# Optimization experiments

Measured on AMD Instinct MI355X. Metric: run time of the kernel, lower is better.

## Reference

```python
import jax, jax.numpy as jnp
import numpy as np

DIM = 768
NUM_HEADS = 12
HEAD_DIM = DIM // NUM_HEADS
HW = 32  # input_size = (32, 32)


def setup_inputs() -> dict:
    key = jax.random.key(0)
    ks = jax.random.split(key, 7)
    return {
        "x": jax.random.normal(ks[0], (8, HW, HW, DIM), dtype=jnp.float32),
        "w_qkv": jax.random.normal(ks[1], (DIM, 3 * DIM), dtype=jnp.float32) * 0.02,
        "b_qkv": jnp.zeros((3 * DIM,), dtype=jnp.float32),
        "w_proj": jax.random.normal(ks[2], (DIM, DIM), dtype=jnp.float32) * 0.02,
        "b_proj": jnp.zeros((DIM,), dtype=jnp.float32),
        "rel_pos_h": jax.random.normal(ks[3], (2 * HW - 1, HEAD_DIM), dtype=jnp.float32) * 0.02,
        "rel_pos_w": jax.random.normal(ks[4], (2 * HW - 1, HEAD_DIM), dtype=jnp.float32) * 0.02,
    }


def _gather_rel_pos(size, rel_pos):
    # q_size == k_size == size, so no resize; index = i - j + (size - 1)
    idx = jnp.arange(size)[:, None] - jnp.arange(size)[None, :] + (size - 1)
    return rel_pos[idx]  # [size, size, head_dim]


def reference(x, w_qkv, b_qkv, w_proj, b_proj, rel_pos_h, rel_pos_w):
    B, H, W, C = x.shape
    nH, D = NUM_HEADS, HEAD_DIM
    scale = D ** -0.5
    S = H * W

    qkv = x.reshape(B, S, C) @ w_qkv + b_qkv          # [B,S,3C]
    qkv = qkv.reshape(B, S, 3, nH, D).transpose(2, 0, 3, 1, 4)  # [3,B,nH,S,D]
    q, k, v = qkv[0], qkv[1], qkv[2]

    attn = jnp.einsum('bnsd,bntd->bnst', q * scale, k)  # [B,nH,S,S]

    # decomposed relative positional bias
    Rh = _gather_rel_pos(H, rel_pos_h)                  # [H,H,D]
    Rw = _gather_rel_pos(W, rel_pos_w)                  # [W,W,D]
    r_q = q.reshape(B, nH, H, W, D)
    rel_h = jnp.einsum('bnhwc,hkc->bnhwk', r_q, Rh)     # [B,nH,H,W,H]
    rel_w = jnp.einsum('bnhwc,wkc->bnhwk', r_q, Rw)     # [B,nH,H,W,W]
    attn = (attn.reshape(B, nH, H, W, H, W)
            + rel_h[..., :, None]
            + rel_w[..., None, :]).reshape(B, nH, S, S)

    attn = jax.nn.softmax(attn, axis=-1)
    out = jnp.einsum('bnst,bntd->bnsd', attn, v)        # [B,nH,S,D]
    out = out.transpose(0, 2, 1, 3).reshape(B, H, W, C)
    return out @ w_proj + b_proj
```

## Files before the change

### kernel.cpp

```cpp
#include <hip/hip_runtime.h>
#include <cstdint>
#include <cstddef>

#define NH 12
#define HDIM 64
#define C_ 768
#define C3 2304
#define SEQ 1024
#define LS 72
#define SMAX 6.0f

typedef short bf16x8_t __attribute__((ext_vector_type(8)));
typedef float f32x4_t __attribute__((ext_vector_type(4)));
typedef unsigned short u16x4_t __attribute__((ext_vector_type(4)));

__device__ __forceinline__ unsigned short bf16_rne(float x) {
    unsigned int u = __float_as_uint(x);
    u += 0x7FFFu + ((u >> 16) & 1u);
    return (unsigned short)(u >> 16);
}
__device__ __forceinline__ float bf16f(unsigned short h) {
    return __uint_as_float(((unsigned int)h) << 16);
}

__device__ __forceinline__ void load_lds16(const unsigned short* g, unsigned short* l) {
    auto gp = (const __attribute__((address_space(1))) unsigned short*)(uintptr_t)g;
    auto lp = (__attribute__((address_space(3))) unsigned short*)(uint32_t)(uintptr_t)l;
    __builtin_amdgcn_global_load_lds(gp, lp, 16, 0, 0);
}

__device__ __forceinline__ int swz(int row, int g) {
    const int pr = row >> 1;
    const int ch = (((row & 1) << 2) | g) ^ (pr & 7);
    return pr * 64 + ch * 8;
}

__global__ __launch_bounds__(256)
void split_kernel(const float* __restrict__ in, unsigned short* __restrict__ hi)
{
    const int i = blockIdx.x * 256 + threadIdx.x;
    float4 v = ((const float4*)in)[i];
    u16x4_t h;
    h.x = bf16_rne(v.x); h.y = bf16_rne(v.y); h.z = bf16_rne(v.z); h.w = bf16_rne(v.w);
    ((u16x4_t*)hi)[i] = h;
}

__global__ __launch_bounds__(256)
void splitT_kernel(const float* __restrict__ W, unsigned short* __restrict__ Thi,
                   unsigned short* __restrict__ Tlo, int Kdim, int Ndim)
{
    __shared__ float tile[32][33];
    const int t = threadIdx.x;
    const int kb = blockIdx.y * 32, nb = blockIdx.x * 32;
    const int lr = t >> 3, lc = (t & 7) * 4;
    *(float4*)&tile[lr][lc] = *(const float4*)&W[(size_t)(kb + lr) * Ndim + nb + lc];
    __syncthreads();
    const float v0 = tile[lc + 0][lr];
    const float v1 = tile[lc + 1][lr];
    const float v2 = tile[lc + 2][lr];
    const float v3 = tile[lc + 3][lr];
    u16x4_t h, l;
    h.x = bf16_rne(v0); l.x = bf16_rne(v0 - bf16f(h.x));
    h.y = bf16_rne(v1); l.y = bf16_rne(v1 - bf16f(h.y));
    h.z = bf16_rne(v2); l.z = bf16_rne(v2 - bf16f(h.z));
    h.w = bf16_rne(v3); l.w = bf16_rne(v3 - bf16f(h.w));
    *(u16x4_t*)&Thi[(size_t)(nb + lr) * Kdim + kb + lc] = h;
    *(u16x4_t*)&Tlo[(size_t)(nb + lr) * Kdim + kb + lc] = l;
}

__global__ __launch_bounds__(256, 2)
void qkvgemm_kernel(const unsigned short* __restrict__ Ahi, const unsigned short* __restrict__ BThi,
                    const float* __restrict__ bias,
                    unsigned short* __restrict__ q_hi, unsigned short* __restrict__ k_hi,
                    unsigned short* __restrict__ v_hi)
{
    constexpr int K = 768;
    __shared__ unsigned short As[4096];
    __shared__ unsigned short Bs[4096];
    const int tid = threadIdx.x;
    const int w = tid >> 6, lane = tid & 63, g = lane >> 4, r = lane & 15;
    const int wr = (w >> 1) * 64, wc = (w & 1) * 64;

    const int bid  = blockIdx.x;
    const int xcd  = bid & 7;
    const int idx  = bid >> 3;
    const int msub = idx & 7;
    const int ntile = idx >> 3;
    const int m0 = (xcd * 8 + msub) * 128;
    const int n0 = ntile * 128;

    int row_[2], gc_[2];
#pragma unroll
    for (int i = 0; i < 2; ++i) {
        const int s = i * 256 + tid;
        const int pr = s >> 3;
        const int u = (s & 7) ^ (pr & 7);
        row_[i] = pr * 2 + (u >> 2);
        gc_[i]  = u & 3;
    }
    const unsigned short* gA0 = Ahi + (size_t)(m0 + row_[0]) * K + gc_[0] * 8;
    const unsigned short* gA1 = Ahi + (size_t)(m0 + row_[1]) * K + gc_[1] * 8;
    const unsigned short* gB0 = BThi + (size_t)(n0 + row_[0]) * K + gc_[0] * 8;
    const unsigned short* gB1 = BThi + (size_t)(n0 + row_[1]) * K + gc_[1] * 8;
    unsigned short* lA0 = As + w * 512;
    unsigned short* lA1 = As + 2048 + w * 512;
    unsigned short* lB0 = Bs + w * 512;
    unsigned short* lB1 = Bs + 2048 + w * 512;

    f32x4_t acc[4][4];
#pragma unroll
    for (int i = 0; i < 4; ++i)
#pragma unroll
        for (int j = 0; j < 4; ++j)
#pragma unroll
            for (int q = 0; q < 4; ++q) acc[i][j][q] = 0.f;

    for (int k0 = 0; k0 < K; k0 += 32) {
        __syncthreads();
        load_lds16(gA0 + k0, lA0);
        load_lds16(gA1 + k0, lA1);
        load_lds16(gB0 + k0, lB0);
        load_lds16(gB1 + k0, lB1);
        __syncthreads();
        bf16x8_t am[4];
#pragma unroll
        for (int i = 0; i < 4; ++i)
            am[i] = *(const bf16x8_t*)&As[swz(wr + 16 * i + r, g)];
#pragma unroll
        for (int j = 0; j < 4; ++j) {
            const bf16x8_t bn = *(const bf16x8_t*)&Bs[swz(wc + 16 * j + r, g)];
#pragma unroll
            for (int i = 0; i < 4; ++i)
                acc[i][j] = __builtin_amdgcn_mfma_f32_16x16x32_bf16(am[i], bn, acc[i][j], 0, 0, 0);
        }
    }

    const int third = n0 >= 1536 ? 2 : (n0 >= 768 ? 1 : 0);
    unsigned short* outH = third == 2 ? v_hi : third == 1 ? k_hi : q_hi;
#pragma unroll
    for (int j = 0; j < 4; ++j) {
        const int n = n0 + wc + 16 * j + r;
        const float bj = bias[n];
        const int nn = n - third * 768;
        const int h = nn >> 6, d = nn & 63;
#pragma unroll
        for (int i = 0; i < 4; ++i) {
            const int m = m0 + wr + 16 * i + 4 * g;
            const int b = m >> 10, t = m & 1023;
            const size_t hb = ((size_t)(b * NH + h)) << 16;
            unsigned short* dh = outH + hb + (size_t)t * 64 + d;
#pragma unroll
            for (int q = 0; q < 4; ++q)
                dh[(size_t)q * 64] = bf16_rne(acc[i][j][q] + bj);
        }
    }
}

template<int N>
__global__ __launch_bounds__(256, 2)
void gemm_mfma_kernel(const unsigned short* __restrict__ Ahi, const unsigned short* __restrict__ Alo,
                      const unsigned short* __restrict__ BThi, const unsigned short* __restrict__ BTlo,
                      const float* __restrict__ bias, float* __restrict__ C)
{
    constexpr int K = 768;
    __shared__ unsigned short As[128 * LS];
    __shared__ unsigned short Bs[128 * LS];
    const int tid = threadIdx.x;
    const int w = tid >> 6, lane = tid & 63, g = lane >> 4, r = lane & 15;
    const int wr = (w >> 1) * 64, wc = (w & 1) * 64;

    const int bid  = blockIdx.x;
    const int xcd  = bid & 7;
    const int idx  = bid >> 3;
    const int msub = idx & 7;
    const int ntile = idx >> 3;
    const int m0 = (xcd * 8 + msub) * 128;
    const int n0 = ntile * 128;

    const int srow = tid >> 1, sh = (tid & 1) * 16;

    const unsigned short* aH = Ahi + (size_t)(m0 + srow) * K + sh;
    const unsigned short* aL = Alo + (size_t)(m0 + srow) * K + sh;
    const unsigned short* bH = BThi + (size_t)(n0 + srow) * K + sh;
    const unsigned short* bL = BTlo + (size_t)(n0 + srow) * K + sh;

    f32x4_t acc[4][4];
#pragma unroll
    for (int i = 0; i < 4; ++i)
#pragma unroll
        for (int j = 0; j < 4; ++j)
#pragma unroll
            for (int q = 0; q < 4; ++q) acc[i][j][q] = 0.f;

    for (int k0 = 0; k0 < K; k0 += 32) {
        bf16x8_t va0 = *(const bf16x8_t*)(aH + k0);
        bf16x8_t va1 = *(const bf16x8_t*)(aH + k0 + 8);
        bf16x8_t wa0 = *(const bf16x8_t*)(aL + k0);
        bf16x8_t wa1 = *(const bf16x8_t*)(aL + k0 + 8);
        bf16x8_t vb0 = *(const bf16x8_t*)(bH + k0);
        bf16x8_t vb1 = *(const bf16x8_t*)(bH + k0 + 8);
        bf16x8_t wb0 = *(const bf16x8_t*)(bL + k0);
        bf16x8_t wb1 = *(const bf16x8_t*)(bL + k0 + 8);
        __syncthreads();
        *(bf16x8_t*)&As[srow * LS + sh]          = va0;
        *(bf16x8_t*)&As[srow * LS + sh + 8]      = va1;
        *(bf16x8_t*)&As[srow * LS + 32 + sh]     = wa0;
        *(bf16x8_t*)&As[srow * LS + 32 + sh + 8] = wa1;
        *(bf16x8_t*)&Bs[srow * LS + sh]          = vb0;
        *(bf16x8_t*)&Bs[srow * LS + sh + 8]      = vb1;
        *(bf16x8_t*)&Bs[srow * LS + 32 + sh]     = wb0;
        *(bf16x8_t*)&Bs[srow * LS + 32 + sh + 8] = wb1;
        __syncthreads();
        bf16x8_t amh[4], aml[4];
#pragma unroll
        for (int i = 0; i < 4; ++i) {
            amh[i] = *(const bf16x8_t*)&As[(wr + 16 * i + r) * LS + 8 * g];
            aml[i] = *(const bf16x8_t*)&As[(wr + 16 * i + r) * LS + 32 + 8 * g];
        }
#pragma unroll
        for (int j = 0; j < 4; ++j) {
            bf16x8_t bnh = *(const bf16x8_t*)&Bs[(wc + 16 * j + r) * LS + 8 * g];
            bf16x8_t bnl = *(const bf16x8_t*)&Bs[(wc + 16 * j + r) * LS + 32 + 8 * g];
#pragma unroll
            for (int i = 0; i < 4; ++i) {
                acc[i][j] = __builtin_amdgcn_mfma_f32_16x16x32_bf16(amh[i], bnh, acc[i][j], 0, 0, 0);
                acc[i][j] = __builtin_amdgcn_mfma_f32_16x16x32_bf16(amh[i], bnl, acc[i][j], 0, 0, 0);
                acc[i][j] = __builtin_amdgcn_mfma_f32_16x16x32_bf16(aml[i], bnh, acc[i][j], 0, 0, 0);
            }
        }
    }

#pragma unroll
    for (int j = 0; j < 4; ++j) {
        const float bj = bias[n0 + wc + 16 * j + r];
#pragma unroll
        for (int i = 0; i < 4; ++i) {
            float* Cp = C + (size_t)(m0 + wr + 16 * i + 4 * g) * N + n0 + wc + 16 * j + r;
#pragma unroll
            for (int q = 0; q < 4; ++q)
                Cp[(size_t)q * N] = acc[i][j][q] + bj;
        }
    }
}

__global__ __launch_bounds__(256)
void relcat_kernel(const float* __restrict__ rel_h, const float* __restrict__ rel_w,
                   unsigned short* __restrict__ relcat)
{
    const int i = blockIdx.x * 256 + threadIdx.x;
    if (i >= 2016) return;
    const int j = i * 4;
    const int row = j >> 6, col = j & 63;
    const float* src = row < 63 ? &rel_h[row * 64 + col] : &rel_w[(row - 63) * 64 + col];
    const float4 v = *(const float4*)src;
    u16x4_t h;
    h.x = bf16_rne(v.x); h.y = bf16_rne(v.y); h.z = bf16_rne(v.z); h.w = bf16_rne(v.w);
    *(u16x4_t*)&relcat[j] = h;
}

__global__ __launch_bounds__(256, 4)
void relgemm_kernel(const unsigned short* __restrict__ qhi, const unsigned short* __restrict__ relcat,
                    unsigned short* __restrict__ G)
{
    __shared__ unsigned short bs[128 * LS];
    const int tid = threadIdx.x;
    const int sb = blockIdx.x, bh = blockIdx.y;
    const int w = tid >> 6, lane = tid & 63, g = lane >> 4, r = lane & 15;
    const size_t hb = (size_t)bh << 16;

    {
        const int row = tid >> 1, c32 = (tid & 1) * 32;
        if (row < 126) {
#pragma unroll
            for (int e = 0; e < 4; ++e)
                *(bf16x8_t*)&bs[row * LS + c32 + 8 * e] =
                    *(const bf16x8_t*)&relcat[row * 64 + c32 + 8 * e];
        } else {
            const bf16x8_t z = {0,0,0,0,0,0,0,0};
#pragma unroll
            for (int e = 0; e < 4; ++e)
                *(bf16x8_t*)&bs[row * LS + c32 + 8 * e] = z;
        }
    }
    bf16x8_t aq[2][2];
#pragma unroll
    for (int i = 0; i < 2; ++i)
#pragma unroll
        for (int c = 0; c < 2; ++c)
            aq[i][c] = *(const bf16x8_t*)(qhi + hb + (size_t)(sb * 128 + w * 32 + 16 * i + r) * 64 + c * 32 + 8 * g);
    __syncthreads();

    f32x4_t acc[2][8];
#pragma unroll
    for (int i = 0; i < 2; ++i)
#pragma unroll
        for (int fj = 0; fj < 8; ++fj)
#pragma unroll
            for (int q = 0; q < 4; ++q) acc[i][fj][q] = 0.f;

#pragma unroll
    for (int c = 0; c < 2; ++c)
#pragma unroll
        for (int fj = 0; fj < 8; ++fj) {
            const bf16x8_t brel = *(const bf16x8_t*)&bs[(16 * fj + r) * LS + c * 32 + 8 * g];
#pragma unroll
            for (int i = 0; i < 2; ++i)
                acc[i][fj] = __builtin_amdgcn_mfma_f32_16x16x32_bf16(aq[i][c], brel, acc[i][fj], 0, 0, 0);
        }

    unsigned short* Gb = G + (((size_t)bh << 10) + sb * 128 + w * 32) * 128;
#pragma unroll
    for (int i = 0; i < 2; ++i)
#pragma unroll
        for (int reg = 0; reg < 4; ++reg) {
            unsigned short* Gr = Gb + (size_t)(16 * i + 4 * g + reg) * 128 + r;
#pragma unroll
            for (int fj = 0; fj < 8; ++fj)
                Gr[16 * fj] = bf16_rne(acc[i][fj][reg]);
        }
}

__global__ __launch_bounds__(256, 3)
void attn7_kernel(const unsigned short* __restrict__ qhi,
                  const unsigned short* __restrict__ khi,
                  const unsigned short* __restrict__ vhi,
                  const unsigned short* __restrict__ G,
                  unsigned short* __restrict__ outh, unsigned short* __restrict__ outl)
{
    __shared__ unsigned short ksh[2 * 64 * LS];
    __shared__ unsigned short vsh[2 * 64 * LS];
    __shared__ unsigned short psh[64 * 64];

    const int tid  = threadIdx.x;
    const int bh   = blockIdx.x;
    const int s0   = blockIdx.y * 64;
    const int w    = tid >> 6;
    const int lane = tid & 63;
    const int g    = lane >> 4;
    const int r    = lane & 15;
    const size_t hb = (size_t)bh << 16;

    bf16x8_t aq[2];
#pragma unroll
    for (int c = 0; c < 2; ++c)
        aq[c] = *(const bf16x8_t*)(qhi + hb + (size_t)(s0 + w * 16 + r) * 64 + c * 32 + 8 * g);

    const unsigned short* Grow[4];
    int qcb[4];
    float bw[4][2];
#pragma unroll
    for (int reg = 0; reg < 4; ++reg) {
        const int row = s0 + w * 16 + 4 * g + reg;
        Grow[reg] = G + (((size_t)bh << 10) + row) * 128;
        qcb[reg] = (row >> 5) + 31;
        const int iw = row & 31;
#pragma unroll
        for (int jh = 0; jh < 2; ++jh)
            bw[reg][jh] = bf16f(Grow[reg][94 + iw - 16 * jh - r]);
    }

    f32x4_t oacc[4];
    float lsum[4];
#pragma unroll
    for (int i = 0; i < 4; ++i) {
        lsum[i] = 0.f;
#pragma unroll
        for (int j = 0; j < 4; ++j) oacc[i][j] = 0.f;
    }

    const int krow = tid >> 2, kc16 = (tid & 3) * 16;
    const int tb = (tid >> 4) * 4, d0 = (tid & 15) * 4;

    {
        const unsigned short* kh = khi + hb + (size_t)krow * 64 + kc16;
        const bf16x8_t a0 = *(const bf16x8_t*)kh;
        const bf16x8_t a1 = *(const bf16x8_t*)(kh + 8);
        u16x4_t rv[4];
#pragma unroll
        for (int i = 0; i < 4; ++i)
            rv[i] = *(const u16x4_t*)(vhi + hb + (size_t)(tb + i) * 64 + d0);
        *(bf16x8_t*)&ksh[krow * LS + kc16]     = a0;
        *(bf16x8_t*)&ksh[krow * LS + kc16 + 8] = a1;
#pragma unroll
        for (int c2 = 0; c2 < 4; ++c2) {
            u16x4_t th;
            th.x = rv[0][c2]; th.y = rv[1][c2]; th.z = rv[2][c2]; th.w = rv[3][c2];
            *(u16x4_t*)&vsh[(d0 + c2) * LS + tb] = th;
        }
    }
    __syncthreads();

    int cur = 0;
    for (int t0 = 0; t0 < SEQ; t0 += 64) {
        const int co = cur * 64 * LS;
        const int tn = (t0 + 64 < SEQ) ? t0 + 64 : t0;
        bf16x8_t nk0, nk1;
        u16x4_t nv[4];
        {
            const unsigned short* kh = khi + hb + (size_t)(tn + krow) * 64 + kc16;
            nk0 = *(const bf16x8_t*)kh;
            nk1 = *(const bf16x8_t*)(kh + 8);
#pragma unroll
            for (int i = 0; i < 4; ++i)
                nv[i] = *(const u16x4_t*)(vhi + hb + (size_t)(tn + tb + i) * 64 + d0);
        }

        f32x4_t sacc[4];
#pragma unroll
        for (int fj = 0; fj < 4; ++fj)
#pragma unroll
            for (int j = 0; j < 4; ++j) sacc[fj][j] = 0.f;
#pragma unroll
        for (int c = 0; c < 2; ++c)
#pragma unroll
            for (int fj = 0; fj < 4; ++fj) {
                const bf16x8_t bkh = *(const bf16x8_t*)&ksh[co + (16 * fj + r) * LS + c * 32 + 8 * g];
                sacc[fj] = __builtin_amdgcn_mfma_f32_16x16x32_bf16(aq[c], bkh, sacc[fj], 0, 0, 0);
            }

        const int kh0 = t0 >> 5;
        float bh0[4], bh1[4];
#pragma unroll
        for (int reg = 0; reg < 4; ++reg) {
            bh0[reg] = bf16f(Grow[reg][qcb[reg] - kh0]) - SMAX;
            bh1[reg] = bf16f(Grow[reg][qcb[reg] - kh0 - 1]) - SMAX;
        }
#pragma unroll
        for (int fj = 0; fj < 4; ++fj)
#pragma unroll
            for (int reg = 0; reg < 4; ++reg) {
                const float s = fmaf(sacc[fj][reg], 0.125f,
                                     ((fj >> 1) ? bh1[reg] : bh0[reg]) + bw[reg][fj & 1]);
                const float e = __expf(s);
                sacc[fj][reg] = e;
                lsum[reg] += e;
            }

#pragma unroll
        for (int fj = 0; fj < 4; ++fj)
#pragma unroll
            for (int reg = 0; reg < 4; ++reg) {
                const int row = w * 16 + 4 * g + reg;
                const int addr = row * 64 + (((2 * fj + (r >> 3)) ^ (row & 7)) << 3) + (r & 7);
                psh[addr] = bf16_rne(sacc[fj][reg]);
            }
        asm volatile("s_waitcnt lgkmcnt(0)" ::: "memory");
        __builtin_amdgcn_sched_barrier(0);

#pragma unroll
        for (int c = 0; c < 2; ++c) {
            const int prow = w * 16 + r;
            const int paddr = prow * 64 + (((4 * c + g) ^ (prow & 7)) << 3);
            const bf16x8_t aph = *(const bf16x8_t*)&psh[paddr];
#pragma unroll
            for (int fd = 0; fd < 4; ++fd) {
                const bf16x8_t bvh = *(const bf16x8_t*)&vsh[co + (16 * fd + r) * LS + c * 32 + 8 * g];
                oacc[fd] = __builtin_amdgcn_mfma_f32_16x16x32_bf16(aph, bvh, oacc[fd], 0, 0, 0);
            }
        }

        const int no = (cur ^ 1) * 64 * LS;
        *(bf16x8_t*)&ksh[no + krow * LS + kc16]     = nk0;
        *(bf16x8_t*)&ksh[no + krow * LS + kc16 + 8] = nk1;
#pragma unroll
        for (int c2 = 0; c2 < 4; ++c2) {
            u16x4_t th;
            th.x = nv[0][c2]; th.y = nv[1][c2]; th.z = nv[2][c2]; th.w = nv[3][c2];
            *(u16x4_t*)&vsh[no + (d0 + c2) * LS + tb] = th;
        }
        __syncthreads();
        cur ^= 1;
    }

    const int b = bh / NH, h = bh - (bh / NH) * NH;
#pragma unroll
    for (int reg = 0; reg < 4; ++reg) {
        float rs = lsum[reg];
#pragma unroll
        for (int off = 1; off < 16; off <<= 1) rs += __shfl_xor(rs, off);
        const float rinv = 1.f / rs;
        const int qrow = s0 + w * 16 + 4 * g + reg;
        unsigned short* oph = outh + ((size_t)b * SEQ + qrow) * C_ + h * HDIM;
        unsigned short* opl = outl + ((size_t)b * SEQ + qrow) * C_ + h * HDIM;
#pragma unroll
        for (int fd = 0; fd < 4; ++fd) {
            const float v = oacc[fd][reg] * rinv;
            const unsigned short hv = bf16_rne(v);
            oph[16 * fd + r] = hv;
            opl[16 * fd + r] = bf16_rne(v - bf16f(hv));
        }
    }
}

extern "C" void kernel_launch(void* const* d_in, const int* in_sizes, int n_in,
                              void* d_out, int out_size, void* d_ws, size_t ws_size,
                              hipStream_t stream) {
    (void)in_sizes; (void)n_in; (void)out_size; (void)ws_size;
    const float* x      = (const float*)d_in[0];
    const float* w_qkv  = (const float*)d_in[1];
    const float* b_qkv  = (const float*)d_in[2];
    const float* w_proj = (const float*)d_in[3];
    const float* b_proj = (const float*)d_in[4];
    const float* rel_h  = (const float*)d_in[5];
    const float* rel_w  = (const float*)d_in[6];
    float* out = (float*)d_out;

    char* base = (char*)d_ws;
    unsigned short* xhi    = (unsigned short*)(base + 0);
    unsigned short* xlo    = (unsigned short*)(base + 12582912);
    unsigned short* wqh    = (unsigned short*)(base + 25165824);
    unsigned short* wql    = (unsigned short*)(base + 28704768);
    unsigned short* wph    = (unsigned short*)(base + 32243712);
    unsigned short* wpl    = (unsigned short*)(base + 33423360);
    unsigned short* qhi    = (unsigned short*)(base + 34603008);
    unsigned short* relcat = (unsigned short*)(base + 47185920);
    unsigned short* khi    = (unsigned short*)(base + 59768832);
    unsigned short* vhi    = (unsigned short*)(base + 84934656);
    unsigned short* G      = (unsigned short*)(base + 110100480);
    unsigned short* ohif   = xhi;
    unsigned short* olo    = xlo;

    split_kernel<<<6144, 256, 0, stream>>>(x, xhi);
    {
        dim3 gq(C3 / 32, C_ / 32);
        splitT_kernel<<<gq, 256, 0, stream>>>(w_qkv, wqh, wql, C_, C3);
        dim3 gp(C_ / 32, C_ / 32);
        splitT_kernel<<<gp, 256, 0, stream>>>(w_proj, wph, wpl, C_, C_);
        relcat_kernel<<<8, 256, 0, stream>>>(rel_h, rel_w, relcat);
    }
    qkvgemm_kernel<<<1152, 256, 0, stream>>>(xhi, wqh, b_qkv, qhi, khi, vhi);
    {
        dim3 grid(8, 96);
        relgemm_kernel<<<grid, 256, 0, stream>>>(qhi, relcat, G);
    }
    {
        dim3 grid(96, SEQ / 64);
        attn7_kernel<<<grid, 256, 0, stream>>>(qhi, khi, vhi, G, ohif, olo);
    }
    gemm_mfma_kernel<C_><<<384, 256, 0, stream>>>(ohif, olo, wph, wpl, b_proj, out);
}
```

Baseline: 183.4 us.

## Process 128 query rows per attention block to reuse K/V tiles

```diff
diff --git a/kernel.cpp b/kernel.cpp
--- a/kernel.cpp
+++ b/kernel.cpp
@@ -8,7 +8,9 @@
 #define C3 2304
 #define SEQ 1024
 #define LS 72
+#define LSV 76
 #define SMAX 6.0f
+#define LOG2E 1.4426950408889634f
 
 typedef short bf16x8_t __attribute__((ext_vector_type(8)));
 typedef float f32x4_t __attribute__((ext_vector_type(4)));
@@ -321,52 +323,57 @@
 }
 
 __global__ __launch_bounds__(256, 3)
-void attn7_kernel(const unsigned short* __restrict__ qhi,
+void attn8_kernel(const unsigned short* __restrict__ qhi,
                   const unsigned short* __restrict__ khi,
                   const unsigned short* __restrict__ vhi,
                   const unsigned short* __restrict__ G,
                   unsigned short* __restrict__ outh, unsigned short* __restrict__ outl)
 {
     __shared__ unsigned short ksh[2 * 64 * LS];
-    __shared__ unsigned short vsh[2 * 64 * LS];
+    __shared__ unsigned short vsh[2 * 64 * LSV];
     __shared__ unsigned short psh[64 * 64];
 
     const int tid  = threadIdx.x;
     const int bh   = blockIdx.x;
-    const int s0   = blockIdx.y * 64;
+    const int s0   = blockIdx.y * 128;
     const int w    = tid >> 6;
     const int lane = tid & 63;
     const int g    = lane >> 4;
     const int r    = lane & 15;
     const size_t hb = (size_t)bh << 16;
 
-    bf16x8_t aq[2];
-#pragma unroll
-    for (int c = 0; c < 2; ++c)
-        aq[c] = *(const bf16x8_t*)(qhi + hb + (size_t)(s0 + w * 16 + r) * 64 + c * 32 + 8 * g);
-
-    const unsigned short* Grow[4];
-    int qcb[4];
-    float bw[4][2];
-#pragma unroll
-    for (int reg = 0; reg < 4; ++reg) {
-        const int row = s0 + w * 16 + 4 * g + reg;
-        Grow[reg] = G + (((size_t)bh << 10) + row) * 128;
-        qcb[reg] = (row >> 5) + 31;
-        const int iw = row & 31;
-#pragma unroll
-        for (int jh = 0; jh < 2; ++jh)
-            bw[reg][jh] = bf16f(Grow[reg][94 + iw - 16 * jh - r]);
-    }
-
-    f32x4_t oacc[4];
-    float lsum[4];
-#pragma unroll
-    for (int i = 0; i < 4; ++i) {
-        lsum[i] = 0.f;
-#pragma unroll
-        for (int j = 0; j < 4; ++j) oacc[i][j] = 0.f;
-    }
+    bf16x8_t aq[2][2];
+#pragma unroll
+    for (int i = 0; i < 2; ++i)
+#pragma unroll
+        for (int c = 0; c < 2; ++c)
+            aq[i][c] = *(const bf16x8_t*)(qhi + hb + (size_t)(s0 + w * 32 + 16 * i + r) * 64 + c * 32 + 8 * g);
+
+    const unsigned short* Gbh = G + ((size_t)bh << 17);
+    int gidx[2][4];
+    float bw[2][4][2];
+#pragma unroll
+    for (int i = 0; i < 2; ++i)
+#pragma unroll
+        for (int reg = 0; reg < 4; ++reg) {
+            const int row = s0 + w * 32 + 16 * i + 4 * g + reg;
+            gidx[i][reg] = row * 128 + (row >> 5) + 31;
+            const int iw = row & 31;
+#pragma unroll
+            for (int jh = 0; jh < 2; ++jh)
+                bw[i][reg][jh] = bf16f(Gbh[row * 128 + 94 + iw - 16 * jh - r]) * LOG2E;
+        }
+
+    f32x4_t oacc[2][4];
+    float lsum[2][4];
+#pragma unroll
+    for (int i = 0; i < 2; ++i)
+#pragma unroll
+        for (int reg = 0; reg < 4; ++reg) {
+            lsum[i][reg] = 0.f;
+#pragma unroll
+            for (int q = 0; q < 4; ++q) oacc[i][reg][q] = 0.f;
+        }
 
     const int krow = tid >> 2, kc16 = (tid & 3) * 16;
     const int tb = (tid >> 4) * 4, d0 = (tid & 15) * 4;
@@ -385,14 +392,15 @@
         for (int c2 = 0; c2 < 4; ++c2) {
             u16x4_t th;
             th.x = rv[0][c2]; th.y = rv[1][c2]; th.z = rv[2][c2]; th.w = rv[3][c2];
-            *(u16x4_t*)&vsh[(d0 + c2) * LS + tb] = th;
+            *(u16x4_t*)&vsh[(d0 + c2) * LSV + tb] = th;
         }
     }
     __syncthreads();
 
     int cur = 0;
     for (int t0 = 0; t0 < SEQ; t0 += 64) {
-        const int co = cur * 64 * LS;
+        const int cok = cur * 64 * LS;
+        const int cov = cur * 64 * LSV;
         const int tn = (t0 + 64 < SEQ) ? t0 + 64 : t0;
         bf16x8_t nk0, nk1;
         u16x4_t nv[4];
@@ -405,68 +413,77 @@
                 nv[i] = *(const u16x4_t*)(vhi + hb + (size_t)(tn + tb + i) * 64 + d0);
         }
 
-        f32x4_t sacc[4];
-#pragma unroll
-        for (int fj = 0; fj < 4; ++fj)
-#pragma unroll
-            for (int j = 0; j < 4; ++j) sacc[fj][j] = 0.f;
+        f32x4_t sacc[2][4];
+#pragma unroll
+        for (int i = 0; i < 2; ++i)
+#pragma unroll
+            for (int fj = 0; fj < 4; ++fj)
+#pragma unroll
+                for (int q = 0; q < 4; ++q) sacc[i][fj][q] = 0.f;
 #pragma unroll
         for (int c = 0; c < 2; ++c)
 #pragma unroll
             for (int fj = 0; fj < 4; ++fj) {
-                const bf16x8_t bkh = *(const bf16x8_t*)&ksh[co + (16 * fj + r) * LS + c * 32 + 8 * g];
-                sacc[fj] = __builtin_amdgcn_mfma_f32_16x16x32_bf16(aq[c], bkh, sacc[fj], 0, 0, 0);
+                const bf16x8_t bkh = *(const bf16x8_t*)&ksh[cok + (16 * fj + r) * LS + c * 32 + 8 * g];
+                sacc[0][fj] = __builtin_amdgcn_mfma_f32_16x16x32_bf16(aq[0][c], bkh, sacc[0][fj], 0, 0, 0);
+                sacc[1][fj] = __builtin_amdgcn_mfma_f32_16x16x32_bf16(aq[1][c], bkh, sacc[1][fj], 0, 0, 0);
             }
 
         const int kh0 = t0 >> 5;
-        float bh0[4], bh1[4];
-#pragma unroll
-        for (int reg = 0; reg < 4; ++reg) {
-            bh0[reg] = bf16f(Grow[reg][qcb[reg] - kh0]) - SMAX;
-            bh1[reg] = bf16f(Grow[reg][qcb[reg] - kh0 - 1]) - SMAX;
-        }
-#pragma unroll
-        for (int fj = 0; fj < 4; ++fj)
+#pragma unroll
+        for (int i = 0; i < 2; ++i) {
+            float bh0[4], bh1[4];
 #pragma unroll
             for (int reg = 0; reg < 4; ++reg) {
-                const float s = fmaf(sacc[fj][reg], 0.125f,
-                                     ((fj >> 1) ? bh1[reg] : bh0[reg]) + bw[reg][fj & 1]);
-                const float e = __expf(s);
-                sacc[fj][reg] = e;
-                lsum[reg] += e;
+                bh0[reg] = (bf16f(Gbh[gidx[i][reg] - kh0])     - SMAX) * LOG2E;
+                bh1[reg] = (bf16f(Gbh[gidx[i][reg] - kh0 - 1]) - SMAX) * LOG2E;
             }
-
-#pragma unroll
-        for (int fj = 0; fj < 4; ++fj)
-#pragma unroll
-            for (int reg = 0; reg < 4; ++reg) {
-                const int row = w * 16 + 4 * g + reg;
-                const int addr = row * 64 + (((2 * fj + (r >> 3)) ^ (row & 7)) << 3) + (r & 7);
-                psh[addr] = bf16_rne(sacc[fj][reg]);
+#pragma unroll
+            for (int fj = 0; fj < 4; ++fj)
+#pragma unroll
+                for (int reg = 0; reg < 4; ++reg) {
+                    const float s = fmaf(sacc[i][fj][reg], 0.125f * LOG2E,
+                                         ((fj >> 1) ? bh1[reg] : bh0[reg]) + bw[i][reg][fj & 1]);
+                    const float e = exp2f(s);
+                    sacc[i][fj][reg] = e;
+                    lsum[i][reg] += e;
+                }
+        }
+
+#pragma unroll
+        for (int i = 0; i < 2; ++i) {
+#pragma unroll
+            for (int fj = 0; fj < 4; ++fj)
+#pragma unroll
+                for (int reg = 0; reg < 4; ++reg) {
+                    const int rowp = w * 16 + 4 * g + reg;
+                    const int addr = rowp * 64 + (((2 * fj + (r >> 3)) ^ (rowp & 7)) << 3) + (r & 7);
+                    psh[addr] = bf16_rne(sacc[i][fj][reg]);
+                }
+            asm volatile("s_waitcnt lgkmcnt(0)" ::: "memory");
+            __builtin_amdgcn_sched_barrier(0);
+#pragma unroll
+            for (int c = 0; c < 2; ++c) {
+                const int prow = w * 16 + r;
+                const int paddr = prow * 64 + (((4 * c + g) ^ (prow & 7)) << 3);
+                const bf16x8_t aph = *(const bf16x8_t*)&psh[paddr];
+#pragma unroll
+                for (int fd = 0; fd < 4; ++fd) {
+                    const bf16x8_t bvh = *(const bf16x8_t*)&vsh[cov + (16 * fd + r) * LSV + c * 32 + 8 * g];
+                    oacc[i][fd] = __builtin_amdgcn_mfma_f32_16x16x32_bf16(aph, bvh, oacc[i][fd], 0, 0, 0);
+                }
             }
-        asm volatile("s_waitcnt lgkmcnt(0)" ::: "memory");
-        __builtin_amdgcn_sched_barrier(0);
-
-#pragma unroll
-        for (int c = 0; c < 2; ++c) {
-            const int prow = w * 16 + r;
-            const int paddr = prow * 64 + (((4 * c + g) ^ (prow & 7)) << 3);
-            const bf16x8_t aph = *(const bf16x8_t*)&psh[paddr];
-#pragma unroll
-            for (int fd = 0; fd < 4; ++fd) {
-                const bf16x8_t bvh = *(const bf16x8_t*)&vsh[co + (16 * fd + r) * LS + c * 32 + 8 * g];
-                oacc[fd] = __builtin_amdgcn_mfma_f32_16x16x32_bf16(aph, bvh, oacc[fd], 0, 0, 0);
-            }
-        }
-
-        const int no = (cur ^ 1) * 64 * LS;
-        *(bf16x8_t*)&ksh[no + krow * LS + kc16]     = nk0;
-        *(bf16x8_t*)&ksh[no + krow * LS + kc16 + 8] = nk1;
+        }
+
+        const int nok = (cur ^ 1) * 64 * LS;
+        const int nov = (cur ^ 1) * 64 * LSV;
+        *(bf16x8_t*)&ksh[nok + krow * LS + kc16]     = nk0;
+        *(bf16x8_t*)&ksh[nok + krow * LS + kc16 + 8] = nk1;
 #pragma unroll
         for (int c2 = 0; c2 < 4; ++c2) {
             u16x4_t th;
             th.x = nv[0][c2]; th.y = nv[1][c2]; th.z = nv[2][c2]; th.w = nv[3][c2];
-            *(u16x4_t*)&vsh[no + (d0 + c2) * LS + tb] = th;
+            *(u16x4_t*)&vsh[nov + (d0 + c2) * LSV + tb] = th;
         }
         __syncthreads();
         cur ^= 1;
@@ -474,22 +491,24 @@
 
     const int b = bh / NH, h = bh - (bh / NH) * NH;
 #pragma unroll
-    for (int reg = 0; reg < 4; ++reg) {
-        float rs = lsum[reg];
-#pragma unroll
-        for (int off = 1; off < 16; off <<= 1) rs += __shfl_xor(rs, off);
-        const float rinv = 1.f / rs;
-        const int qrow = s0 + w * 16 + 4 * g + reg;
-        unsigned short* oph = outh + ((size_t)b * SEQ + qrow) * C_ + h * HDIM;
-        unsigned short* opl = outl + ((size_t)b * SEQ + qrow) * C_ + h * HDIM;
-#pragma unroll
-        for (int fd = 0; fd < 4; ++fd) {
-            const float v = oacc[fd][reg] * rinv;
-            const unsigned short hv = bf16_rne(v);
-            oph[16 * fd + r] = hv;
-            opl[16 * fd + r] = bf16_rne(v - bf16f(hv));
-        }
-    }
+    for (int i = 0; i < 2; ++i)
+#pragma unroll
+        for (int reg = 0; reg < 4; ++reg) {
+            float rs = lsum[i][reg];
+#pragma unroll
+            for (int off = 1; off < 16; off <<= 1) rs += __shfl_xor(rs, off);
+            const float rinv = 1.f / rs;
+            const int qrow = s0 + w * 32 + 16 * i + 4 * g + reg;
+            unsigned short* oph = outh + ((size_t)b * SEQ + qrow) * C_ + h * HDIM;
+            unsigned short* opl = outl + ((size_t)b * SEQ + qrow) * C_ + h * HDIM;
+#pragma unroll
+            for (int fd = 0; fd < 4; ++fd) {
+                const float v = oacc[i][fd][reg] * rinv;
+                const unsigned short hv = bf16_rne(v);
+                oph[16 * fd + r] = hv;
+                opl[16 * fd + r] = bf16_rne(v - bf16f(hv));
+            }
+        }
 }
 
 extern "C" void kernel_launch(void* const* d_in, const int* in_sizes, int n_in,
@@ -534,8 +553,8 @@
         relgemm_kernel<<<grid, 256, 0, stream>>>(qhi, relcat, G);
     }
     {
-        dim3 grid(96, SEQ / 64);
-        attn7_kernel<<<grid, 256, 0, stream>>>(qhi, khi, vhi, G, ohif, olo);
+        dim3 grid(96, SEQ / 128);
+        attn8_kernel<<<grid, 256, 0, stream>>>(qhi, khi, vhi, G, ohif, olo);
     }
     gemm_mfma_kernel<C_><<<384, 256, 0, stream>>>(ohif, olo, wph, wpl, b_proj, out);
 }
```

New measurement: 267.2 us. 1.46x slower.
